# Performance work log

Measured on AMD Instinct MI355X. Metric: run time of the kernel, lower is better.

Reference implementation:

```python
import jax, jax.numpy as jnp
import numpy as np

EPS_LOG = 1e-08   # module's eps added inside the log
EPS_PD = 1e-06    # torch.nn.PairwiseDistance default eps (added to the difference)


def setup_inputs() -> dict:
    key = jax.random.key(0)
    x = jax.random.normal(key, (16384, 512), dtype=jnp.float32)
    return {"x": x}


def reference(x):
    n = x.shape[0]
    # Pairwise dot products; mask diagonal with -1 (as in the torch code)
    dots = jnp.matmul(x, x.T)  # [n, n]
    dots = jnp.where(jnp.eye(n, dtype=bool), jnp.float32(-1.0), dots)
    I = jnp.argmax(dots, axis=1)  # nearest neighbor index per row (no grad)
    # torch PairwiseDistance(2): ||x1 - x2 + eps||_2 with eps=1e-6
    diff = x - x[I] + EPS_PD  # [n, d]
    rho = jnp.sqrt(jnp.sum(diff * diff, axis=1))  # [n]
    loss = -jnp.mean(jnp.log(rho + EPS_LOG))
    return loss
```

## Files before the change

kernel.cpp:

```cpp
#include <hip/hip_runtime.h>
#include <stdint.h>

#define N_ROWS 16384
#define DIM    512

typedef float v4f __attribute__((ext_vector_type(4)));
typedef unsigned long long u64;
typedef unsigned char u8;

__device__ __forceinline__ unsigned fkey(float f) {
    unsigned u = __float_as_uint(f);
    return (u & 0x80000000u) ? ~u : (u | 0x80000000u);
}

__device__ __forceinline__ void gload_lds16(const void* g, void* l) {
    __builtin_amdgcn_global_load_lds(
        (const __attribute__((address_space(1))) unsigned int*)g,
        (__attribute__((address_space(3))) unsigned int*)l,
        16, 0, 0);
}

__global__ __launch_bounds__(256)
void convert_fp8_kernel(const float* __restrict__ x, unsigned* __restrict__ x8,
                        u64* __restrict__ table) {
    int tid    = blockIdx.x * blockDim.x + threadIdx.x;
    int stride = gridDim.x * blockDim.x;
    if (tid < N_ROWS) table[tid] = 0;
    const float4* x4 = (const float4*)x;
    const int n4 = (N_ROWS * DIM) / 4;
    for (int i = tid; i < n4; i += stride) {
        float4 v = x4[i];
        int b = __builtin_amdgcn_cvt_pk_fp8_f32(v.x, v.y, 0, false);
        b     = __builtin_amdgcn_cvt_pk_fp8_f32(v.z, v.w, b, true);
        x8[i] = (unsigned)b;
    }
}

__global__ __launch_bounds__(256)
void argmax_dots_kernel(const u8* __restrict__ xb, u64* __restrict__ table) {
    __shared__ __attribute__((aligned(16))) u8 ldsA[128 * 128];
    __shared__ __attribute__((aligned(16))) u8 ldsB[128 * 128];

    const int u = blockIdx.x >> 6;
    const int p = blockIdx.x & 63;
    const int rT = (u <= p) ? (127 - p) : p;
    const int cT = (u <= p) ? (127 - u) : (u - 1);

    const int t      = threadIdx.x;
    const int lane   = t & 63;
    const int wave   = t >> 6;
    const int lane15 = lane & 15;
    const int quad   = lane >> 4;
    const int rh = wave >> 1;
    const int ch = wave & 1;

    const int rowBase = rT * 128;
    const int colBase = cT * 128;

    const u8* gA[4];
    const u8* gB[4];
#pragma unroll
    for (int j = 0; j < 4; ++j) {
        const int L   = j * 256 + t;
        const int row = L >> 3;
        const int kc  = (L & 7) ^ (row & 7);
        gA[j] = xb + (size_t)(rowBase + row) * DIM + kc * 16;
        gB[j] = xb + (size_t)(colBase + row) * DIM + kc * 16;
    }
    const int dstOff = wave * 1024;

    const int aBase = (rh * 64 + lane15) * 128 + (quad & 1) * 8;
    const int bBase = (ch * 64 + lane15) * 128 + (quad & 1) * 8;
    int xorK[4];
#pragma unroll
    for (int s = 0; s < 4; ++s)
        xorK[s] = ((2 * s + (quad >> 1)) ^ (lane15 & 7)) << 4;

    v4f acc[4][4];
#pragma unroll
    for (int rf = 0; rf < 4; ++rf)
#pragma unroll
        for (int cf = 0; cf < 4; ++cf) {
            v4f z = {0.f, 0.f, 0.f, 0.f};
            acc[rf][cf] = z;
        }

#pragma unroll
    for (int k = 0; k < 4; ++k) {
        const int kk = k * 128;
#pragma unroll
        for (int j = 0; j < 4; ++j) {
            gload_lds16(gA[j] + kk, (char*)ldsA + j * 4096 + dstOff);
            gload_lds16(gB[j] + kk, (char*)ldsB + j * 4096 + dstOff);
        }
        __syncthreads();

#pragma unroll
        for (int s = 0; s < 4; ++s) {
            const int xs = xorK[s];
            long a8[4], b8[4];
#pragma unroll
            for (int rf = 0; rf < 4; ++rf)
                a8[rf] = *(const long*)(ldsA + aBase + rf * 2048 + xs);
#pragma unroll
            for (int cf = 0; cf < 4; ++cf)
                b8[cf] = *(const long*)(ldsB + bBase + cf * 2048 + xs);
#pragma unroll
            for (int rf = 0; rf < 4; ++rf)
#pragma unroll
                for (int cf = 0; cf < 4; ++cf)
                    acc[rf][cf] = __builtin_amdgcn_mfma_f32_16x16x32_fp8_fp8(
                        a8[rf], b8[cf], acc[rf][cf], 0, 0, 0);
        }
        __syncthreads();
    }

    const int colLane = colBase + ch * 64 + lane15;
#pragma unroll
    for (int rf = 0; rf < 4; ++rf) {
#pragma unroll
        for (int e = 0; e < 4; ++e) {
            const int row = rowBase + rh * 64 + rf * 16 + quad * 4 + e;
            float bv = -3.0e38f;
            int   bc = 0;
#pragma unroll
            for (int cf = 0; cf < 4; ++cf) {
                const float v = acc[rf][cf][e];
                const int col = colLane + cf * 16;
                if (v > bv && col != row) { bv = v; bc = col; }
            }
            u64 packed = ((u64)fkey(bv) << 32) | (unsigned)(~bc);
#pragma unroll
            for (int m = 1; m < 16; m <<= 1) {
                u64 o = __shfl_xor(packed, m, 64);
                if (o > packed) packed = o;
            }
            if (lane15 == 0) atomicMax(&table[row], packed);
        }
    }

    if (rT != cT) {
#pragma unroll
        for (int cf = 0; cf < 4; ++cf) {
            const int col = colLane + cf * 16;
            float bv = -3.0e38f;
            int   br_ = 0;
#pragma unroll
            for (int rf = 0; rf < 4; ++rf)
#pragma unroll
                for (int e = 0; e < 4; ++e) {
                    const float v = acc[rf][cf][e];
                    const int row = rowBase + rh * 64 + rf * 16 + quad * 4 + e;
                    if (v > bv) { bv = v; br_ = row; }
                }
            u64 packed = ((u64)fkey(bv) << 32) | (unsigned)(~br_);
            u64 o = __shfl_xor(packed, 16, 64); if (o > packed) packed = o;
            o     = __shfl_xor(packed, 32, 64); if (o > packed) packed = o;
            if (quad == 0) atomicMax(&table[col], packed);
        }
    }
}

__global__ __launch_bounds__(256)
void rho_loss_kernel(const float* __restrict__ x, const u64* __restrict__ table,
                     float* __restrict__ out) {
    const int lane = threadIdx.x & 63;
    const int wave = threadIdx.x >> 6;
    const int waveGlobal = blockIdx.x * 4 + wave;

    float local = 0.f;
    for (int r8 = 0; r8 < 8; ++r8) {
        const int row = waveGlobal * 8 + r8;
        const u64 packed = table[row];
        const int nb = (int)(~(unsigned)(packed & 0xFFFFFFFFu));

        const float4* xr = (const float4*)(x + (size_t)row * DIM);
        const float4* xn = (const float4*)(x + (size_t)nb  * DIM);
        float s = 0.f;
#pragma unroll
        for (int tt = 0; tt < 2; ++tt) {
            float4 a = xr[lane * 2 + tt];
            float4 b = xn[lane * 2 + tt];
            float d0 = a.x - b.x + 1e-6f;
            float d1 = a.y - b.y + 1e-6f;
            float d2 = a.z - b.z + 1e-6f;
            float d3 = a.w - b.w + 1e-6f;
            s += d0 * d0 + d1 * d1 + d2 * d2 + d3 * d3;
        }
#pragma unroll
        for (int m = 1; m < 64; m <<= 1) s += __shfl_xor(s, m, 64);

        if (lane == 0) {
            float rho = sqrtf(s);
            local += logf(rho + 1e-8f);
        }
    }
    if (lane == 0) atomicAdd(out, -local * (1.0f / 16384.0f));
}

extern "C" void kernel_launch(void* const* d_in, const int* in_sizes, int n_in,
                              void* d_out, int out_size, void* d_ws, size_t ws_size,
                              hipStream_t stream) {
    const float* x = (const float*)d_in[0];

    u8*    xb    = (u8*)d_ws;
    u64*   table = (u64*)((char*)d_ws + (size_t)N_ROWS * DIM);
    float* out   = (float*)d_out;

    hipMemsetAsync(out, 0, sizeof(float), stream);

    convert_fp8_kernel<<<2048, 256, 0, stream>>>(x, (unsigned*)xb, table);
    argmax_dots_kernel<<<8256, 256, 0, stream>>>(xb, table);
    rho_loss_kernel<<<512, 256, 0, stream>>>(x, table, out);
}
```

Measured before the change: 265.3 us.

## Use 256x256 tiles with double-buffered K pipeline in argmax GEMM

The argmax GEMM kernel moves from 128x128 tiles with 4 waves to 256x256 tiles with 8 waves (each wave computing 128x64). K is split into 8 steps of 64 bytes that are double-buffered in LDS, with loads prefetched two stages ahead and explicit vmcnt waits, barriers and setprio around the MFMA bursts. This raises data reuse per LDS byte, cuts the number of blocks and the atomic traffic, and overlaps global loads with compute. In exchange it uses more registers per thread (launch bounds 512,2) and more barriers per K step, which may limit occupancy.

Result: slower. 325.9 us (+22.8%).

```diff
diff --git a/kernel.cpp b/kernel.cpp
--- a/kernel.cpp
+++ b/kernel.cpp
@@ -7,6 +7,8 @@
 typedef float v4f __attribute__((ext_vector_type(4)));
 typedef unsigned long long u64;
 typedef unsigned char u8;
+
+template <int N> struct IC { static constexpr int value = N; };
 
 __device__ __forceinline__ unsigned fkey(float f) {
     unsigned u = __float_as_uint(f);
@@ -36,91 +38,102 @@
     }
 }
 
-__global__ __launch_bounds__(256)
+__global__ __launch_bounds__(512, 2)
 void argmax_dots_kernel(const u8* __restrict__ xb, u64* __restrict__ table) {
-    __shared__ __attribute__((aligned(16))) u8 ldsA[128 * 128];
-    __shared__ __attribute__((aligned(16))) u8 ldsB[128 * 128];
-
-    const int u = blockIdx.x >> 6;
-    const int p = blockIdx.x & 63;
-    const int rT = (u <= p) ? (127 - p) : p;
-    const int cT = (u <= p) ? (127 - u) : (u - 1);
+    __shared__ __attribute__((aligned(16))) u8 ldsA[2][2][8192];
+    __shared__ __attribute__((aligned(16))) u8 ldsB[2][2][8192];
+
+    const int u = blockIdx.x >> 5;
+    const int p = blockIdx.x & 31;
+    const int rT = (u <= p) ? (63 - p) : p;
+    const int cT = (u <= p) ? (63 - u) : (u - 1);
 
     const int t      = threadIdx.x;
     const int lane   = t & 63;
     const int wave   = t >> 6;
     const int lane15 = lane & 15;
     const int quad   = lane >> 4;
-    const int rh = wave >> 1;
-    const int ch = wave & 1;
-
-    const int rowBase = rT * 128;
-    const int colBase = cT * 128;
-
-    const u8* gA[4];
-    const u8* gB[4];
-#pragma unroll
-    for (int j = 0; j < 4; ++j) {
-        const int L   = j * 256 + t;
-        const int row = L >> 3;
-        const int kc  = (L & 7) ^ (row & 7);
-        gA[j] = xb + (size_t)(rowBase + row) * DIM + kc * 16;
-        gB[j] = xb + (size_t)(colBase + row) * DIM + kc * 16;
-    }
-    const int dstOff = wave * 1024;
-
-    const int aBase = (rh * 64 + lane15) * 128 + (quad & 1) * 8;
-    const int bBase = (ch * 64 + lane15) * 128 + (quad & 1) * 8;
-    int xorK[4];
-#pragma unroll
-    for (int s = 0; s < 4; ++s)
-        xorK[s] = ((2 * s + (quad >> 1)) ^ (lane15 & 7)) << 4;
-
-    v4f acc[4][4];
-#pragma unroll
-    for (int rf = 0; rf < 4; ++rf)
+    const int wr     = wave >> 2;
+    const int wc     = wave & 3;
+
+    const int rowBase = rT * 256;
+    const int colBase = cT * 256;
+
+    const int r128 = t >> 2;
+    const int kcs  = (t & 3) ^ ((r128 >> 1) & 3);
+    const u8* sA0 = xb + (size_t)(rowBase +       r128) * DIM + kcs * 16;
+    const u8* sA1 = xb + (size_t)(rowBase + 128 + r128) * DIM + kcs * 16;
+    const u8* sB0 = xb + (size_t)(colBase +       r128) * DIM + kcs * 16;
+    const u8* sB1 = xb + (size_t)(colBase + 128 + r128) * DIM + kcs * 16;
+    const int ldsOff = wave * 1024;
+
+#define STAGE(T) do {                                              \
+        gload_lds16(sA0 + (T) * 64, &ldsA[(T) & 1][0][ldsOff]);    \
+        gload_lds16(sA1 + (T) * 64, &ldsA[(T) & 1][1][ldsOff]);    \
+        gload_lds16(sB0 + (T) * 64, &ldsB[(T) & 1][0][ldsOff]);    \
+        gload_lds16(sB1 + (T) * 64, &ldsB[(T) & 1][1][ldsOff]);    \
+    } while (0)
+
+    const int rdOff = lane15 * 64 + (quad & 1) * 8;
+    int xorK[2];
+#pragma unroll
+    for (int ks = 0; ks < 2; ++ks)
+        xorK[ks] = ((2 * ks + (quad >> 1)) ^ ((lane15 >> 1) & 3)) << 4;
+    const int bcOff = (wc & 1) * 4096;
+
+    v4f acc[8][4];
+#pragma unroll
+    for (int rf = 0; rf < 8; ++rf)
 #pragma unroll
         for (int cf = 0; cf < 4; ++cf) {
             v4f z = {0.f, 0.f, 0.f, 0.f};
             acc[rf][cf] = z;
         }
 
-#pragma unroll
-    for (int k = 0; k < 4; ++k) {
-        const int kk = k * 128;
-#pragma unroll
-        for (int j = 0; j < 4; ++j) {
-            gload_lds16(gA[j] + kk, (char*)ldsA + j * 4096 + dstOff);
-            gload_lds16(gB[j] + kk, (char*)ldsB + j * 4096 + dstOff);
-        }
-        __syncthreads();
-
-#pragma unroll
-        for (int s = 0; s < 4; ++s) {
-            const int xs = xorK[s];
-            long a8[4], b8[4];
-#pragma unroll
-            for (int rf = 0; rf < 4; ++rf)
-                a8[rf] = *(const long*)(ldsA + aBase + rf * 2048 + xs);
+    STAGE(0);
+    STAGE(1);
+
+    auto ktile = [&](auto TC) {
+        constexpr int T  = TC.value;
+        constexpr int WN = (T < 7) ? 4 : 0;
+        asm volatile("s_waitcnt vmcnt(%0)" :: "n"(WN) : "memory");
+        __builtin_amdgcn_s_barrier();
+        const u8* A = &ldsA[T & 1][wr][0];
+        const u8* B = &ldsB[T & 1][wc >> 1][0];
+#pragma unroll
+        for (int ks = 0; ks < 2; ++ks) {
+            long a8[8], b8[4];
+#pragma unroll
+            for (int rf = 0; rf < 8; ++rf)
+                a8[rf] = *(const long*)(A + rf * 1024 + rdOff + xorK[ks]);
 #pragma unroll
             for (int cf = 0; cf < 4; ++cf)
-                b8[cf] = *(const long*)(ldsB + bBase + cf * 2048 + xs);
-#pragma unroll
-            for (int rf = 0; rf < 4; ++rf)
+                b8[cf] = *(const long*)(B + bcOff + cf * 1024 + rdOff + xorK[ks]);
+            __builtin_amdgcn_s_barrier();
+            asm volatile("s_waitcnt lgkmcnt(0)" ::: "memory");
+            __builtin_amdgcn_sched_barrier(0);
+            __builtin_amdgcn_s_setprio(1);
+#pragma unroll
+            for (int rf = 0; rf < 8; ++rf)
 #pragma unroll
                 for (int cf = 0; cf < 4; ++cf)
                     acc[rf][cf] = __builtin_amdgcn_mfma_f32_16x16x32_fp8_fp8(
                         a8[rf], b8[cf], acc[rf][cf], 0, 0, 0);
-        }
-        __syncthreads();
-    }
-
-    const int colLane = colBase + ch * 64 + lane15;
-#pragma unroll
-    for (int rf = 0; rf < 4; ++rf) {
+            __builtin_amdgcn_s_setprio(0);
+            __builtin_amdgcn_s_barrier();
+        }
+        if constexpr (T < 6) STAGE(T + 2);
+    };
+    ktile(IC<0>{}); ktile(IC<1>{}); ktile(IC<2>{}); ktile(IC<3>{});
+    ktile(IC<4>{}); ktile(IC<5>{}); ktile(IC<6>{}); ktile(IC<7>{});
+#undef STAGE
+
+    const int colLane = colBase + wc * 64 + lane15;
+#pragma unroll
+    for (int rf = 0; rf < 8; ++rf) {
 #pragma unroll
         for (int e = 0; e < 4; ++e) {
-            const int row = rowBase + rh * 64 + rf * 16 + quad * 4 + e;
+            const int row = rowBase + wr * 128 + rf * 16 + quad * 4 + e;
             float bv = -3.0e38f;
             int   bc = 0;
 #pragma unroll
@@ -143,14 +156,14 @@
 #pragma unroll
         for (int cf = 0; cf < 4; ++cf) {
             const int col = colLane + cf * 16;
-            float bv = -3.0e38f;
+            float bv  = -3.0e38f;
             int   br_ = 0;
 #pragma unroll
-            for (int rf = 0; rf < 4; ++rf)
+            for (int rf = 0; rf < 8; ++rf)
 #pragma unroll
                 for (int e = 0; e < 4; ++e) {
                     const float v = acc[rf][cf][e];
-                    const int row = rowBase + rh * 64 + rf * 16 + quad * 4 + e;
+                    const int row = rowBase + wr * 128 + rf * 16 + quad * 4 + e;
                     if (v > bv) { bv = v; br_ = row; }
                 }
             u64 packed = ((u64)fkey(bv) << 32) | (unsigned)(~br_);
@@ -210,6 +223,6 @@
     hipMemsetAsync(out, 0, sizeof(float), stream);
 
     convert_fp8_kernel<<<2048, 256, 0, stream>>>(x, (unsigned*)xb, table);
-    argmax_dots_kernel<<<8256, 256, 0, stream>>>(xb, table);
+    argmax_dots_kernel<<<2080, 512, 0, stream>>>(xb, table);
     rho_loss_kernel<<<512, 256, 0, stream>>>(x, table, out);
 }
```
